# Optimization experiments

Measured on AMD Instinct MI355X. Metric: run time of the kernel, lower is better.

The kernel has to match this reference:

```python
import jax, jax.numpy as jnp
import numpy as np

H = 60.0  # self.h
C = jnp.array([10665991.0, 27000000.0, 7953253.0], dtype=jnp.float32)  # self.c (9e6*3 = 27e6)


def setup_inputs() -> dict:
    key = jax.random.key(0)
    k1, k2, k3 = jax.random.split(key, 3)
    B, T = 8192, 1024
    # room temperatures in Kelvin, strictly positive (model uses 1/x)
    x0 = 280.0 + 20.0 * jax.random.uniform(k1, (B, 3), dtype=jnp.float32)
    u = jax.random.uniform(k2, (B, T, 8), dtype=jnp.float32)
    # col 0: external temperature ~[250,300] K; cols 1..7: positive power/irradiation
    u = u.at[:, :, 0].set(250.0 + 50.0 * u[:, :, 0])
    u = u.at[:, :, 1:].multiply(1000.0)
    # 14 scalar log-conductance params: [l12, l23, le1..3, ls1..3, lh1..3, lc1..3]
    lam = 0.1 * jax.random.normal(k3, (14,), dtype=jnp.float32)
    return {"x0": x0, "u": u, "lam": lam}


def _forward(x0, u, lam):
    e = jnp.exp(lam)
    e12, e23 = e[0], e[1]
    ee, es, eh, ec = e[2:5], e[5:8], e[8:11], e[11:14]  # each [3]

    def step(x, ut):  # x: [B,3], ut: [B,8]
        inv = 1.0 / x
        d12 = inv[:, 0] - inv[:, 1]
        d23 = inv[:, 1] - inv[:, 2]
        # A @ x^T, with A's only nonzeros at (0,1),(1,0),(1,2),(2,1)
        Ax = jnp.stack([
            e12 * d12 * x[:, 1],
            -e12 * d12 * x[:, 0] + e23 * d23 * x[:, 2],
            -e23 * d23 * x[:, 1],
        ], axis=-1)  # [B,3]
        u0 = ut[:, 0:1]  # external temperature
        # B @ u_t: external exchange + solar + per-room heating (u2..4) + cooling (u5..7)
        Bu = (ee * (inv - 1.0 / u0) * u0
              + es * ut[:, 1:2]
              + eh * ut[:, 2:5]
              + ec * ut[:, 5:8])  # [B,3]
        x_new = x * jnp.exp(H * (Ax + Bu) / C)
        return x_new, x_new

    # loop runs for T-1 steps using u[:, t] for t = 0..T-2
    u_seq = jnp.swapaxes(u[:, :-1, :], 0, 1)  # [T-1, B, 8]
    _, xs = jax.lax.scan(step, x0, u_seq)
    preds_rest = jnp.swapaxes(xs, 0, 1)  # [B, T-1, 3]
    # rows where the NEXT step's external temp is ~0 are flagged with -1
    invalid = u[:, 1:, 0] < 1e-6  # [B, T-1]
    preds_rest = jnp.where(invalid[..., None], jnp.float32(-1.0), preds_rest)
    return jnp.concatenate([x0[:, None, :], preds_rest], axis=1)  # [B, T, 3]


def reference(x0, u, lam):
    return _forward(x0, u, lam)
```

## Files before the change

kernel.cpp:

```cpp
#include <hip/hip_runtime.h>


namespace {
constexpr int T = 1024;
constexpr int ROWS_PER_BLK = 8;
constexpr int NBLK = T / ROWS_PER_BLK;
}

__global__ __launch_bounds__(64, 1) void bm_fwd(
    const float* __restrict__ x0p,
    const float* __restrict__ up,
    const float* __restrict__ lamp,
    float* __restrict__ outp)
{
    const int b = blockIdx.x * 64 + threadIdx.x;

    float e[14];
#pragma unroll
    for (int i = 0; i < 14; ++i) e[i] = expf(lamp[i]);
    const float e12 = e[0], e23 = e[1];
    const float ee0 = e[2], ee1 = e[3], ee2 = e[4];
    const float es0 = e[5], es1 = e[6], es2 = e[7];
    const float eh0 = e[8], eh1 = e[9], eh2 = e[10];
    const float ec0 = e[11], ec1 = e[12], ec2 = e[13];

    const float hc0 = 60.0f / 10665991.0f;
    const float hc1 = 60.0f / 27000000.0f;
    const float hc2 = 60.0f / 7953253.0f;

    float X0 = x0p[3 * b + 0];
    float X1 = x0p[3 * b + 1];
    float X2 = x0p[3 * b + 2];

    const float4* __restrict__ ub = (const float4*)(up + (size_t)b * (T * 8));
    float* __restrict__ ob = outp + (size_t)b * (T * 3);

    float4 A[2 * ROWS_PER_BLK], B[2 * ROWS_PER_BLK];

    auto loadblk = [&](float4* buf, int j) {
        const float4* src = ub + j * (2 * ROWS_PER_BLK);
#pragma unroll
        for (int i = 0; i < 2 * ROWS_PER_BLK; ++i) buf[i] = src[i];
    };

    auto step = [&](const float4& p, const float4& q, int s, bool check) {
        if (check) {
            const bool bad = (p.x < 1e-6f);
            ob[3 * s + 0] = bad ? -1.0f : X0;
            ob[3 * s + 1] = bad ? -1.0f : X1;
            ob[3 * s + 2] = bad ? -1.0f : X2;
        } else {
            ob[0] = X0; ob[1] = X1; ob[2] = X2;
        }
        const float i0 = __builtin_amdgcn_rcpf(X0);
        const float i1 = __builtin_amdgcn_rcpf(X1);
        const float i2 = __builtin_amdgcn_rcpf(X2);
        const float iu = __builtin_amdgcn_rcpf(p.x);
        const float d12 = i0 - i1;
        const float d23 = i1 - i2;
        const float t12 = e12 * d12;
        const float t23 = e23 * d23;
        const float a0 = t12 * X1;
        const float a1 = t23 * X2 - t12 * X0;
        const float a2 = -(t23 * X1);
        const float b0 = ee0 * (i0 - iu) * p.x + es0 * p.y + eh0 * p.z + ec0 * q.y;
        const float b1 = ee1 * (i1 - iu) * p.x + es1 * p.y + eh1 * p.w + ec1 * q.z;
        const float b2 = ee2 * (i2 - iu) * p.x + es2 * p.y + eh2 * q.x + ec2 * q.w;
        X0 = X0 * __expf(hc0 * (a0 + b0));
        X1 = X1 * __expf(hc1 * (a1 + b1));
        X2 = X2 * __expf(hc2 * (a2 + b2));
    };

    auto procblk = [&](const float4* buf, int j, bool first) {
#pragma unroll
        for (int i = 0; i < ROWS_PER_BLK; ++i) {
            const int s = j * ROWS_PER_BLK + i;
            step(buf[2 * i], buf[2 * i + 1], s, !(first && i == 0));
        }
    };

    loadblk(A, 0);
    loadblk(B, 1);
    procblk(A, 0, true);
    for (int j = 1; j < NBLK - 1; j += 2) {
        loadblk(A, j + 1);
        procblk(B, j, false);
        loadblk(B, j + 2);
        procblk(A, j + 1, false);
    }
#pragma unroll
    for (int i = 0; i < ROWS_PER_BLK - 1; ++i) {
        const int s = (NBLK - 1) * ROWS_PER_BLK + i;
        step(B[2 * i], B[2 * i + 1], s, true);
    }
    {
        const bool bad = (B[2 * (ROWS_PER_BLK - 1)].x < 1e-6f);
        ob[3 * (T - 1) + 0] = bad ? -1.0f : X0;
        ob[3 * (T - 1) + 1] = bad ? -1.0f : X1;
        ob[3 * (T - 1) + 2] = bad ? -1.0f : X2;
    }
}

extern "C" void kernel_launch(void* const* d_in, const int* in_sizes, int n_in,
                              void* d_out, int out_size, void* d_ws, size_t ws_size,
                              hipStream_t stream) {
    const float* x0  = (const float*)d_in[0];
    const float* u   = (const float*)d_in[1];
    const float* lam = (const float*)d_in[2];
    float* out = (float*)d_out;

    const int B = in_sizes[0] / 3;
    dim3 grid(B / 64), block(64);
    hipLaunchKernelGGL(bm_fwd, grid, block, 0, stream, x0, u, lam, out);
}
```

Before: 487.4 us.

## Split each chain across 8 lanes with coalesced row loads and lane broadcast

Each batch chain is now handled by 8 cooperating lanes instead of one thread. Every lane loads one timestep row per 8-step block, so global loads and stores are coalesced. The inputs are broadcast across the group with ds_bpermute, and all 8 lanes run the recurrence redundantly while each lane stores only its own row. The input-only terms are precomputed per row, and exp is replaced with exp2 using pre-scaled constants. This raises thread count and memory-level parallelism well above the previous 128 single-wave blocks, at the cost of 8x redundant math and extra cross-lane shuffles.

```diff
diff --git a/kernel.cpp b/kernel.cpp
--- a/kernel.cpp
+++ b/kernel.cpp
@@ -1,19 +1,32 @@
 #include <hip/hip_runtime.h>
 
 
+#if __has_builtin(__builtin_amdgcn_exp2f)
+#define EXP2F(x) __builtin_amdgcn_exp2f(x)
+#else
+#define EXP2F(x) __expf((x) * 0.69314718056f)
+#endif
+
 namespace {
 constexpr int T = 1024;
-constexpr int ROWS_PER_BLK = 8;
-constexpr int NBLK = T / ROWS_PER_BLK;
+constexpr int NBLK = T / 8;
+constexpr float LOG2E = 1.4426950408889634f;
 }
 
-__global__ __launch_bounds__(64, 1) void bm_fwd(
+__device__ __forceinline__ float bcast8(float v, int idx) {
+    return __int_as_float(__builtin_amdgcn_ds_bpermute(idx, __float_as_int(v)));
+}
+
+__global__ __launch_bounds__(256, 1) void bm_fwd(
     const float* __restrict__ x0p,
     const float* __restrict__ up,
     const float* __restrict__ lamp,
     float* __restrict__ outp)
 {
-    const int b = blockIdx.x * 64 + threadIdx.x;
+    const int tid   = blockIdx.x * 256 + threadIdx.x;
+    const int chain = tid >> 3;
+    const int phase = tid & 7;
+    const int idx_base = (threadIdx.x & 56) << 2;
 
     float e[14];
 #pragma unroll
@@ -24,81 +37,82 @@
     const float eh0 = e[8], eh1 = e[9], eh2 = e[10];
     const float ec0 = e[11], ec1 = e[12], ec2 = e[13];
 
-    const float hc0 = 60.0f / 10665991.0f;
-    const float hc1 = 60.0f / 27000000.0f;
-    const float hc2 = 60.0f / 7953253.0f;
+    const float hc0 = (60.0f / 10665991.0f) * LOG2E;
+    const float hc1 = (60.0f / 27000000.0f) * LOG2E;
+    const float hc2 = (60.0f / 7953253.0f) * LOG2E;
 
-    float X0 = x0p[3 * b + 0];
-    float X1 = x0p[3 * b + 1];
-    float X2 = x0p[3 * b + 2];
+    float X0 = x0p[3 * chain + 0];
+    float X1 = x0p[3 * chain + 1];
+    float X2 = x0p[3 * chain + 2];
 
-    const float4* __restrict__ ub = (const float4*)(up + (size_t)b * (T * 8));
-    float* __restrict__ ob = outp + (size_t)b * (T * 3);
+    const float4* __restrict__ ub = (const float4*)(up + (size_t)chain * (T * 8));
+    float* __restrict__ ob = outp + (size_t)chain * (T * 3);
 
-    float4 A[2 * ROWS_PER_BLK], B[2 * ROWS_PER_BLK];
+    float4 A0, A1, B0, B1;
 
-    auto loadblk = [&](float4* buf, int j) {
-        const float4* src = ub + j * (2 * ROWS_PER_BLK);
-#pragma unroll
-        for (int i = 0; i < 2 * ROWS_PER_BLK; ++i) buf[i] = src[i];
+    auto loadA = [&](int j) {
+        const float4* s = ub + (size_t)(8 * j + phase) * 2;
+        A0 = s[0]; A1 = s[1];
+    };
+    auto loadB = [&](int j) {
+        const float4* s = ub + (size_t)(8 * j + phase) * 2;
+        B0 = s[0]; B1 = s[1];
     };
 
-    auto step = [&](const float4& p, const float4& q, int s, bool check) {
-        if (check) {
-            const bool bad = (p.x < 1e-6f);
-            ob[3 * s + 0] = bad ? -1.0f : X0;
-            ob[3 * s + 1] = bad ? -1.0f : X1;
-            ob[3 * s + 2] = bad ? -1.0f : X2;
-        } else {
-            ob[0] = X0; ob[1] = X1; ob[2] = X2;
+    auto procblk = [&](const float4& r0, const float4& r1, int j, bool first) {
+        const float u0 = r0.x;
+        const float Pk0 = fmaf(ec0, r1.y, fmaf(eh0, r0.z, fmaf(es0, r0.y, -ee0)));
+        const float Pk1 = fmaf(ec1, r1.z, fmaf(eh1, r0.w, fmaf(es1, r0.y, -ee1)));
+        const float Pk2 = fmaf(ec2, r1.w, fmaf(eh2, r1.x, fmaf(es2, r0.y, -ee2)));
+
+        float W[8], Q0[8], Q1[8], Q2[8];
+#pragma unroll
+        for (int i = 0; i < 8; ++i) {
+            const int idx = idx_base + (i << 2);
+            W[i]  = bcast8(u0, idx);
+            Q0[i] = bcast8(Pk0, idx);
+            Q1[i] = bcast8(Pk1, idx);
+            Q2[i] = bcast8(Pk2, idx);
         }
-        const float i0 = __builtin_amdgcn_rcpf(X0);
-        const float i1 = __builtin_amdgcn_rcpf(X1);
-        const float i2 = __builtin_amdgcn_rcpf(X2);
-        const float iu = __builtin_amdgcn_rcpf(p.x);
-        const float d12 = i0 - i1;
-        const float d23 = i1 - i2;
-        const float t12 = e12 * d12;
-        const float t23 = e23 * d23;
-        const float a0 = t12 * X1;
-        const float a1 = t23 * X2 - t12 * X0;
-        const float a2 = -(t23 * X1);
-        const float b0 = ee0 * (i0 - iu) * p.x + es0 * p.y + eh0 * p.z + ec0 * q.y;
-        const float b1 = ee1 * (i1 - iu) * p.x + es1 * p.y + eh1 * p.w + ec1 * q.z;
-        const float b2 = ee2 * (i2 - iu) * p.x + es2 * p.y + eh2 * q.x + ec2 * q.w;
-        X0 = X0 * __expf(hc0 * (a0 + b0));
-        X1 = X1 * __expf(hc1 * (a1 + b1));
-        X2 = X2 * __expf(hc2 * (a2 + b2));
+
+        float O0 = 0.0f, O1 = 0.0f, O2 = 0.0f;
+#pragma unroll
+        for (int i = 0; i < 8; ++i) {
+            const bool bad = (W[i] < 1e-6f) && !(first && i == 0);
+            if (phase == i) {
+                O0 = bad ? -1.0f : X0;
+                O1 = bad ? -1.0f : X1;
+                O2 = bad ? -1.0f : X2;
+            }
+            const float i0 = __builtin_amdgcn_rcpf(X0);
+            const float i1 = __builtin_amdgcn_rcpf(X1);
+            const float i2 = __builtin_amdgcn_rcpf(X2);
+            const float t12 = e12 * (i0 - i1);
+            const float t23 = e23 * (i1 - i2);
+            const float b0 = fmaf(ee0, W[i] * i0, Q0[i]);
+            const float b1 = fmaf(ee1, W[i] * i1, Q1[i]);
+            const float b2 = fmaf(ee2, W[i] * i2, Q2[i]);
+            const float z0 = fmaf(t12, X1, b0);
+            const float z1 = fmaf(t23, X2, fmaf(-t12, X0, b1));
+            const float z2 = fmaf(-t23, X1, b2);
+            X0 *= EXP2F(hc0 * z0);
+            X1 *= EXP2F(hc1 * z1);
+            X2 *= EXP2F(hc2 * z2);
+        }
+        float* o = ob + (size_t)(8 * j + phase) * 3;
+        o[0] = O0; o[1] = O1; o[2] = O2;
     };
 
-    auto procblk = [&](const float4* buf, int j, bool first) {
-#pragma unroll
-        for (int i = 0; i < ROWS_PER_BLK; ++i) {
-            const int s = j * ROWS_PER_BLK + i;
-            step(buf[2 * i], buf[2 * i + 1], s, !(first && i == 0));
-        }
-    };
-
-    loadblk(A, 0);
-    loadblk(B, 1);
-    procblk(A, 0, true);
+    loadA(0);
+    loadB(1);
+    procblk(A0, A1, 0, true);
     for (int j = 1; j < NBLK - 1; j += 2) {
-        loadblk(A, j + 1);
-        procblk(B, j, false);
-        loadblk(B, j + 2);
-        procblk(A, j + 1, false);
+        loadA(j + 1);
+        procblk(B0, B1, j, false);
+        loadB(j + 2);
+        procblk(A0, A1, j + 1, false);
     }
-#pragma unroll
-    for (int i = 0; i < ROWS_PER_BLK - 1; ++i) {
-        const int s = (NBLK - 1) * ROWS_PER_BLK + i;
-        step(B[2 * i], B[2 * i + 1], s, true);
-    }
-    {
-        const bool bad = (B[2 * (ROWS_PER_BLK - 1)].x < 1e-6f);
-        ob[3 * (T - 1) + 0] = bad ? -1.0f : X0;
-        ob[3 * (T - 1) + 1] = bad ? -1.0f : X1;
-        ob[3 * (T - 1) + 2] = bad ? -1.0f : X2;
-    }
+    procblk(B0, B1, NBLK - 1, false);
 }
 
 extern "C" void kernel_launch(void* const* d_in, const int* in_sizes, int n_in,
@@ -110,6 +124,7 @@
     float* out = (float*)d_out;
 
     const int B = in_sizes[0] / 3;
-    dim3 grid(B / 64), block(64);
+    const int threads = B * 8;
+    dim3 grid(threads / 256), block(256);
     hipLaunchKernelGGL(bm_fwd, grid, block, 0, stream, x0, u, lam, out);
 }
```

Measured after the change: 436.7 us. -10.4%, faster.
